# Performance work log

Hardware: AMD Instinct MI355X
Metric: run time of the kernel (lower is better)

## Reference

```python
import jax, jax.numpy as jnp
import numpy as np

N_JOINT = 12
INPUT_DIM = 4
BATCH = 524288


def _skew(w):
    z = jnp.zeros((), w.dtype)
    return jnp.stack([jnp.stack([z, -w[2], w[1]]),
                      jnp.stack([w[2], z, -w[0]]),
                      jnp.stack([-w[1], w[0], z])])


def _srodrigues(twist6, q):
    # twist6: (6,) = [rho; omega]; q: (B,) joint values -> (B,4,4) screw exponential
    rho, omega = twist6[:3], twist6[3:]
    wn = jnp.sqrt(jnp.sum(omega * omega) + 1e-12)
    u, ru = omega / wn, rho / wn
    th = q * wn                                   # (B,)
    K = _skew(u)
    K2 = K @ K
    I3 = jnp.eye(3, dtype=twist6.dtype)
    s = jnp.sin(th)[:, None, None]
    c = (1.0 - jnp.cos(th))[:, None, None]
    t = (th - jnp.sin(th))[:, None, None]
    R = I3 + s * K + c * K2                       # (B,3,3) Rodrigues rotation
    G = th[:, None, None] * I3 + c * K + t * K2   # (B,3,3) translation part
    p = G @ ru                                    # (B,3)
    top = jnp.concatenate([R, p[:, :, None]], axis=2)  # (B,3,4)
    bot = jnp.broadcast_to(jnp.array([0.0, 0.0, 0.0, 1.0], twist6.dtype), (q.shape[0], 1, 4))
    return jnp.concatenate([top, bot], axis=1)


def _rpy2r(rpy):
    r, p, y = rpy[0], rpy[1], rpy[2]
    cr, sr = jnp.cos(r), jnp.sin(r)
    cp, sp = jnp.cos(p), jnp.sin(p)
    cy, sy = jnp.cos(y), jnp.sin(y)
    return jnp.stack([
        jnp.stack([cy * cp, cy * sp * sr - sy * cr, cy * sp * cr + sy * sr]),
        jnp.stack([sy * cp, sy * sp * sr + cy * cr, sy * sp * cr - cy * sr]),
        jnp.stack([-sp, cp * sr, cp * cr])])


def _pr2t(p, rpy):
    R = _rpy2r(rpy)
    top = jnp.concatenate([R, p[:, None]], axis=1)          # (3,4)
    bot = jnp.array([[0.0, 0.0, 0.0, 1.0]], dtype=p.dtype)  # (1,4)
    return jnp.concatenate([top, bot], axis=0)


def setup_inputs() -> dict:
    key = jax.random.key(0)
    ks = jax.random.split(key, 16)
    dims = [INPUT_DIM, 16, 32, 64, 32, N_JOINT]
    inp = {"motor_control": jax.random.normal(ks[0], (BATCH, INPUT_DIM), dtype=jnp.float32)}
    for i in range(5):
        fan_in, fan_out = dims[i], dims[i + 1]
        lim = float(np.sqrt(6.0 / (fan_in + fan_out)))
        inp[f"W{i+1}"] = jax.random.uniform(ks[2 * i + 1], (fan_out, fan_in), minval=-lim, maxval=lim, dtype=jnp.float32)
        inp[f"b{i+1}"] = jax.random.uniform(ks[2 * i + 2], (fan_out,), minval=-0.1, maxval=0.1, dtype=jnp.float32)
    inp["twist"] = jax.random.uniform(ks[11], (N_JOINT, 6, 1), minval=-1.0, maxval=1.0, dtype=jnp.float32)
    inp["init_p"] = jax.random.uniform(ks[12], (1, 3, 1), minval=-1.0, maxval=1.0, dtype=jnp.float32)
    inp["init_rpy"] = jax.random.uniform(ks[13], (1, 3, 1), minval=-1.0, maxval=1.0, dtype=jnp.float32)
    return inp


def reference(motor_control, W1, b1, W2, b2, W3, b3, W4, b4, W5, b5, twist, init_p, init_rpy):
    # q_layer MLP (ReLU after every layer, including the last)
    h = jax.nn.relu(motor_control @ W1.T + b1)
    h = jax.nn.relu(h @ W2.T + b2)
    h = jax.nn.relu(h @ W3.T + b3)
    h = jax.nn.relu(h @ W4.T + b4)
    q = jax.nn.relu(h @ W5.T + b5)  # (B, n_joint)
    B = q.shape[0]
    eye4 = jnp.broadcast_to(jnp.eye(4, dtype=q.dtype), (B, 4, 4))

    def step(carry, xs):
        tw, qj = xs
        return carry @ _srodrigues(tw, qj), None

    out, _ = jax.lax.scan(step, eye4, (twist[:, :, 0], q.T))
    T0 = _pr2t(init_p[0, :, 0], init_rpy[0, :, 0])
    return out @ T0
```

## Files before the change

### kernel.cpp

```cpp
#include <hip/hip_runtime.h>
#include <math.h>

#define BATCH 524288
#define NJ 12

#define WOFF 256
#define BOFF 5632

typedef _Float16 half4 __attribute__((ext_vector_type(4)));
typedef _Float16 half2t __attribute__((ext_vector_type(2)));
typedef float f32x4 __attribute__((ext_vector_type(4)));

#define MFMA16(a, b, c) __builtin_amdgcn_mfma_f32_16x16x16f16((a), (b), (c), 0, 0, 0)

__device__ __forceinline__ f32x4 ld4(const float* p) { return *(const f32x4*)p; }

__device__ __forceinline__ void split4(f32x4 v, half4& h, half4& l) {
    half2t ha = __builtin_bit_cast(half2t, __builtin_amdgcn_cvt_pkrtz(v[0], v[1]));
    half2t hb = __builtin_bit_cast(half2t, __builtin_amdgcn_cvt_pkrtz(v[2], v[3]));
    float r0 = v[0] - (float)ha[0];
    float r1 = v[1] - (float)ha[1];
    float r2 = v[2] - (float)hb[0];
    float r3 = v[3] - (float)hb[1];
    half2t la = __builtin_bit_cast(half2t, __builtin_amdgcn_cvt_pkrtz(r0, r1));
    half2t lb = __builtin_bit_cast(half2t, __builtin_amdgcn_cvt_pkrtz(r2, r3));
    h = half4{ha[0], ha[1], hb[0], hb[1]};
    l = half4{la[0], la[1], lb[0], lb[1]};
}

__device__ __forceinline__ f32x4 relu4(f32x4 v) {
    f32x4 r;
#pragma unroll
    for (int i = 0; i < 4; i++) r[i] = fmaxf(v[i], 0.0f);
    return r;
}

__device__ __forceinline__ void unpack_frag(uint4 u, half4& h, half4& l) {
    uint2 a = make_uint2(u.x, u.y), b = make_uint2(u.z, u.w);
    h = __builtin_bit_cast(half4, a);
    l = __builtin_bit_cast(half4, b);
}

__global__ void precompute_kernel(const float* __restrict__ twist,
                                  const float* __restrict__ init_p,
                                  const float* __restrict__ init_rpy,
                                  const float* __restrict__ W1, const float* __restrict__ b1,
                                  const float* __restrict__ W2, const float* __restrict__ b2,
                                  const float* __restrict__ W3, const float* __restrict__ b3,
                                  const float* __restrict__ W4, const float* __restrict__ b4,
                                  const float* __restrict__ W5, const float* __restrict__ b5,
                                  float* __restrict__ ws) {
    const int lane = threadIdx.x;
    const int qd = lane >> 4, l16 = lane & 15;
    const f32x4 FZ = {0.f, 0.f, 0.f, 0.f};

    if (lane < NJ) {
        int j = lane;
        float rho0 = twist[j*6+0], rho1 = twist[j*6+1], rho2 = twist[j*6+2];
        float w0   = twist[j*6+3], w1   = twist[j*6+4], w2   = twist[j*6+5];
        float wn = sqrtf(w0*w0 + w1*w1 + w2*w2 + 1e-12f);
        float inv = 1.0f / wn;
        float u0 = w0*inv, u1 = w1*inv, u2 = w2*inv;
        float ru0 = rho0*inv, ru1 = rho1*inv, ru2 = rho2*inv;
        float kru0 = u1*ru2 - u2*ru1;
        float kru1 = u2*ru0 - u0*ru2;
        float kru2 = u0*ru1 - u1*ru0;
        float ud = u0*ru0 + u1*ru1 + u2*ru2;
        float* o = ws + j*20;
        o[0] = wn;  o[1] = u0;  o[2] = u1;  o[3] = u2;
        o[4] = ru0; o[5] = ru1; o[6] = ru2;
        o[7] = kru0; o[8] = kru1; o[9] = kru2;
        o[10] = u0*ud - ru0; o[11] = u1*ud - ru1; o[12] = u2*ud - ru2;
        o[13] = u0*u0; o[14] = u0*u1; o[15] = u0*u2;
        o[16] = u1*u1; o[17] = u1*u2; o[18] = u2*u2;
    } else if (lane == NJ) {
        float r = init_rpy[0], p = init_rpy[1], y = init_rpy[2];
        float cr = cosf(r), sr = sinf(r);
        float cp = cosf(p), sp = sinf(p);
        float cy = cosf(y), sy = sinf(y);
        float* o = ws + NJ*20;
        o[0] = cy*cp; o[1] = cy*sp*sr - sy*cr; o[2] = cy*sp*cr + sy*sr;
        o[3] = sy*cp; o[4] = sy*sp*sr + cy*cr; o[5] = sy*sp*cr - cy*sr;
        o[6] = -sp;   o[7] = cp*sr;            o[8] = cp*cr;
        o[9] = init_p[0]; o[10] = init_p[1]; o[11] = init_p[2];
    }

    uint4* wf = (uint4*)(ws + WOFF);
    f32x4* bf = (f32x4*)(ws + BOFF);

    auto pack = [&](f32x4 w) -> uint4 {
        half4 h, l;
#pragma unroll
        for (int i = 0; i < 4; i++) {
            _Float16 hi = (_Float16)w[i];
            h[i] = hi;
            l[i] = (_Float16)(w[i] - (float)hi);
        }
        uint2 uh = __builtin_bit_cast(uint2, h);
        uint2 ul = __builtin_bit_cast(uint2, l);
        return make_uint4(uh.x, uh.y, ul.x, ul.y);
    };

    {
        f32x4 w = ld4(W1 + l16*4);
        wf[0*64 + lane] = pack(qd == 0 ? w : FZ);
    }
    for (int ot = 0; ot < 2; ot++)
        wf[(1+ot)*64 + lane] = pack(ld4(W2 + (ot*16 + l16)*16 + 4*qd));
    for (int ot = 0; ot < 4; ot++)
        for (int kc = 0; kc < 2; kc++)
            wf[(3 + ot*2 + kc)*64 + lane] = pack(ld4(W3 + (ot*16 + l16)*32 + kc*16 + 4*qd));
    for (int ot = 0; ot < 2; ot++)
        for (int kc = 0; kc < 4; kc++)
            wf[(11 + ot*4 + kc)*64 + lane] = pack(ld4(W4 + (ot*16 + l16)*64 + kc*16 + 4*qd));
    {
        int r5 = (l16 < 12) ? l16 : 11;
        for (int kc = 0; kc < 2; kc++) {
            f32x4 w = ld4(W5 + r5*32 + kc*16 + 4*qd);
            wf[(19+kc)*64 + lane] = pack(l16 < 12 ? w : FZ);
        }
    }
    bf[0*64 + lane] = ld4(b1 + 4*qd);
    for (int ot = 0; ot < 2; ot++) bf[(1+ot)*64 + lane] = ld4(b2 + ot*16 + 4*qd);
    for (int ot = 0; ot < 4; ot++) bf[(3+ot)*64 + lane] = ld4(b3 + ot*16 + 4*qd);
    for (int ot = 0; ot < 2; ot++) bf[(7+ot)*64 + lane] = ld4(b4 + ot*16 + 4*qd);
    {
        f32x4 w = ld4(b5 + ((qd < 3) ? 4*qd : 8));
        bf[9*64 + lane] = (qd < 3) ? w : FZ;
    }
}

__global__ __launch_bounds__(256, 3) void fk_kernel(
    const float* __restrict__ mc,
    const float* __restrict__ ws,
    float* __restrict__ out) {
    const int tid = threadIdx.x;
    const int wv = tid >> 6, lane = tid & 63;
    const int qd = lane >> 4, l16 = lane & 15;
    const int wave_base = (blockIdx.x * 4 + wv) * 64;

    const uint4* wf = (const uint4*)(ws + WOFF);
    const f32x4* bf = (const f32x4*)(ws + BOFF);

    __shared__ float qbuf[4][64*13];

    f32x4 xv[4];
#pragma unroll
    for (int d = 0; d < 4; d++) {
        const int row = (d >> 1)*32 + (d & 1)*16 + l16;
        xv[d] = ld4(mc + (size_t)(wave_base + row) * 4);
    }

    const half4 HZ = {(_Float16)0, (_Float16)0, (_Float16)0, (_Float16)0};

    half4 bxh[4], bxl[4];
#pragma unroll
    for (int d = 0; d < 4; d++) {
        split4(xv[d], bxh[d], bxl[d]);
        if (qd != 0) { bxh[d] = HZ; bxl[d] = HZ; }
    }


    half4 g1h[4], g1l[4];
    {
        half4 wh, wl; unpack_frag(wf[0*64 + lane], wh, wl);
        f32x4 bv = bf[0*64 + lane];
#pragma unroll
        for (int d = 0; d < 4; d++) {
            f32x4 acc = bv;
            acc = MFMA16(wh, bxh[d], acc);
            acc = MFMA16(wh, bxl[d], acc);
            acc = MFMA16(wl, bxh[d], acc);
            split4(relu4(acc), g1h[d], g1l[d]);
        }
    }

    half4 g2h[4][2], g2l[4][2];
#pragma unroll
    for (int ot = 0; ot < 2; ot++) {
        half4 wh, wl; unpack_frag(wf[(1+ot)*64 + lane], wh, wl);
        f32x4 bv = bf[(1+ot)*64 + lane];
#pragma unroll
        for (int d = 0; d < 4; d++) {
            f32x4 acc = bv;
            acc = MFMA16(wh, g1h[d], acc);
            acc = MFMA16(wh, g1l[d], acc);
            acc = MFMA16(wl, g1h[d], acc);
            split4(relu4(acc), g2h[d][ot], g2l[d][ot]);
        }
    }

    half4 g3h[4][4], g3l[4][4];
#pragma unroll
    for (int ot = 0; ot < 4; ot++) {
        f32x4 bv = bf[(3+ot)*64 + lane];
        f32x4 acc[4];
#pragma unroll
        for (int d = 0; d < 4; d++) acc[d] = bv;
#pragma unroll
        for (int kc = 0; kc < 2; kc++) {
            half4 wh, wl; unpack_frag(wf[(3 + ot*2 + kc)*64 + lane], wh, wl);
#pragma unroll
            for (int d = 0; d < 4; d++) {
                acc[d] = MFMA16(wh, g2h[d][kc], acc[d]);
                acc[d] = MFMA16(wh, g2l[d][kc], acc[d]);
                acc[d] = MFMA16(wl, g2h[d][kc], acc[d]);
            }
        }
#pragma unroll
        for (int d = 0; d < 4; d++)
            split4(relu4(acc[d]), g3h[d][ot], g3l[d][ot]);
    }

    half4 g4h[4][2], g4l[4][2];
#pragma unroll
    for (int ot = 0; ot < 2; ot++) {
        f32x4 bv = bf[(7+ot)*64 + lane];
        f32x4 acc[4];
#pragma unroll
        for (int d = 0; d < 4; d++) acc[d] = bv;
#pragma unroll
        for (int kc = 0; kc < 4; kc++) {
            half4 wh, wl; unpack_frag(wf[(11 + ot*4 + kc)*64 + lane], wh, wl);
#pragma unroll
            for (int d = 0; d < 4; d++) {
                acc[d] = MFMA16(wh, g3h[d][kc], acc[d]);
                acc[d] = MFMA16(wh, g3l[d][kc], acc[d]);
                acc[d] = MFMA16(wl, g3h[d][kc], acc[d]);
            }
        }
#pragma unroll
        for (int d = 0; d < 4; d++)
            split4(relu4(acc[d]), g4h[d][ot], g4l[d][ot]);
    }

    {
        f32x4 bv = bf[9*64 + lane];
        f32x4 acc[4];
#pragma unroll
        for (int d = 0; d < 4; d++) acc[d] = bv;
#pragma unroll
        for (int kc = 0; kc < 2; kc++) {
            half4 wh, wl; unpack_frag(wf[(19+kc)*64 + lane], wh, wl);
#pragma unroll
            for (int d = 0; d < 4; d++) {
                acc[d] = MFMA16(wh, g4h[d][kc], acc[d]);
                acc[d] = MFMA16(wh, g4l[d][kc], acc[d]);
                acc[d] = MFMA16(wl, g4h[d][kc], acc[d]);
            }
        }
#pragma unroll
        for (int d = 0; d < 4; d++) {
            f32x4 qv = relu4(acc[d]);
            if (qd < 3) {
                const int row = (d >> 1)*32 + (d & 1)*16 + l16;
                float* qb = &qbuf[wv][row*13 + 4*qd];
                qb[0] = qv[0]; qb[1] = qv[1]; qb[2] = qv[2]; qb[3] = qv[3];
            }
        }
    }

    asm volatile("s_waitcnt lgkmcnt(0)" ::: "memory");

    float qq[12];
#pragma unroll
    for (int j = 0; j < 12; j++) qq[j] = qbuf[wv][lane*13 + j];

    const float* jc = ws;
    float M00 = 1.f, M01 = 0.f, M02 = 0.f;
    float M10 = 0.f, M11 = 1.f, M12 = 0.f;
    float M20 = 0.f, M21 = 0.f, M22 = 1.f;
    float v0 = 0.f, v1 = 0.f, v2 = 0.f;

#pragma unroll
    for (int j = 0; j < NJ; j++) {
        const float* c = jc + j*20;
        float wn = c[0];
        float u0 = c[1], u1 = c[2], u2 = c[3];
        float ru0 = c[4], ru1 = c[5], ru2 = c[6];
        float kru0 = c[7], kru1 = c[8], kru2 = c[9];
        float k2ru0 = c[10], k2ru1 = c[11], k2ru2 = c[12];
        float uu00 = c[13], uu01 = c[14], uu02 = c[15];
        float uu11 = c[16], uu12 = c[17], uu22 = c[18];

        float th = qq[j] * wn;
        float s = __sinf(th);
        float cth = __cosf(th);
        float cc = 1.0f - cth;
        float t = th - s;

        float R00 = 1.0f + cc*(uu00 - 1.0f);
        float R01 = cc*uu01 - s*u2;
        float R02 = cc*uu02 + s*u1;
        float R10 = cc*uu01 + s*u2;
        float R11 = 1.0f + cc*(uu11 - 1.0f);
        float R12 = cc*uu12 - s*u0;
        float R20 = cc*uu02 - s*u1;
        float R21 = cc*uu12 + s*u0;
        float R22 = 1.0f + cc*(uu22 - 1.0f);

        float p0 = th*ru0 + cc*kru0 + t*k2ru0;
        float p1 = th*ru1 + cc*kru1 + t*k2ru1;
        float p2 = th*ru2 + cc*kru2 + t*k2ru2;

        float n00 = M00*R00 + M01*R10 + M02*R20;
        float n01 = M00*R01 + M01*R11 + M02*R21;
        float n02 = M00*R02 + M01*R12 + M02*R22;
        float n10 = M10*R00 + M11*R10 + M12*R20;
        float n11 = M10*R01 + M11*R11 + M12*R21;
        float n12 = M10*R02 + M11*R12 + M12*R22;
        float n20 = M20*R00 + M21*R10 + M22*R20;
        float n21 = M20*R01 + M21*R11 + M22*R21;
        float n22 = M20*R02 + M21*R12 + M22*R22;
        v0 += M00*p0 + M01*p1 + M02*p2;
        v1 += M10*p0 + M11*p1 + M12*p2;
        v2 += M20*p0 + M21*p1 + M22*p2;
        M00 = n00; M01 = n01; M02 = n02;
        M10 = n10; M11 = n11; M12 = n12;
        M20 = n20; M21 = n21; M22 = n22;
    }

    const float* t0 = jc + NJ*20;
    float A00 = t0[0], A01 = t0[1], A02 = t0[2];
    float A10 = t0[3], A11 = t0[4], A12 = t0[5];
    float A20 = t0[6], A21 = t0[7], A22 = t0[8];
    float P0  = t0[9], P1  = t0[10], P2 = t0[11];

    float F00 = M00*A00 + M01*A10 + M02*A20;
    float F01 = M00*A01 + M01*A11 + M02*A21;
    float F02 = M00*A02 + M01*A12 + M02*A22;
    float F10 = M10*A00 + M11*A10 + M12*A20;
    float F11 = M10*A01 + M11*A11 + M12*A21;
    float F12 = M10*A02 + M11*A12 + M12*A22;
    float F20 = M20*A00 + M21*A10 + M22*A20;
    float F21 = M20*A01 + M21*A11 + M22*A21;
    float F22 = M20*A02 + M21*A12 + M22*A22;
    float Fv0 = M00*P0 + M01*P1 + M02*P2 + v0;
    float Fv1 = M10*P0 + M11*P1 + M12*P2 + v1;
    float Fv2 = M20*P0 + M21*P1 + M22*P2 + v2;

    const int eo = wave_base + lane;
    float4* o4 = (float4*)(out + (size_t)eo * 16);
    o4[0] = make_float4(F00, F01, F02, Fv0);
    o4[1] = make_float4(F10, F11, F12, Fv1);
    o4[2] = make_float4(F20, F21, F22, Fv2);
    o4[3] = make_float4(0.f, 0.f, 0.f, 1.f);
}

extern "C" void kernel_launch(void* const* d_in, const int* in_sizes, int n_in,
                              void* d_out, int out_size, void* d_ws, size_t ws_size,
                              hipStream_t stream) {
    const float* mc      = (const float*)d_in[0];
    const float* W1      = (const float*)d_in[1];
    const float* b1      = (const float*)d_in[2];
    const float* W2      = (const float*)d_in[3];
    const float* b2      = (const float*)d_in[4];
    const float* W3      = (const float*)d_in[5];
    const float* b3      = (const float*)d_in[6];
    const float* W4      = (const float*)d_in[7];
    const float* b4      = (const float*)d_in[8];
    const float* W5      = (const float*)d_in[9];
    const float* b5      = (const float*)d_in[10];
    const float* twist   = (const float*)d_in[11];
    const float* init_p  = (const float*)d_in[12];
    const float* init_rpy= (const float*)d_in[13];
    float* out = (float*)d_out;
    float* ws  = (float*)d_ws;

    precompute_kernel<<<1, 64, 0, stream>>>(twist, init_p, init_rpy,
                                            W1, b1, W2, b2, W3, b3, W4, b4, W5, b5, ws);
    fk_kernel<<<BATCH / 256, 256, 0, stream>>>(mc, ws, out);
}
```

Measured before the change: 129.6 us.

## Process two elements per lane with packed float2 FK chain math

Each wave now handles 128 batch elements instead of 64: the MLP runs twice in a non-unrolled loop, writing q values into a doubled shared buffer. The forward-kinematics chain then processes two elements per lane using float2 vector types, so the compiler can emit packed FP32 instructions (v_pk_fma_f32) and amortize the per-joint constant loads. The grid is halved and launch bounds lowered to 2 blocks per CU, which raises register and LDS use per wave in exchange for less occupancy.

New measurement: 128.0 us. Within noise of the previous version (-1.2%).

```diff
diff --git a/kernel.cpp b/kernel.cpp
--- a/kernel.cpp
+++ b/kernel.cpp
@@ -10,6 +10,7 @@
 typedef _Float16 half4 __attribute__((ext_vector_type(4)));
 typedef _Float16 half2t __attribute__((ext_vector_type(2)));
 typedef float f32x4 __attribute__((ext_vector_type(4)));
+typedef float f32x2 __attribute__((ext_vector_type(2)));
 
 #define MFMA16(a, b, c) __builtin_amdgcn_mfma_f32_16x16x16f16((a), (b), (c), 0, 0, 0)
 
@@ -130,147 +131,153 @@
     }
 }
 
-__global__ __launch_bounds__(256, 3) void fk_kernel(
+__global__ __launch_bounds__(256, 2) void fk_kernel(
     const float* __restrict__ mc,
     const float* __restrict__ ws,
     float* __restrict__ out) {
     const int tid = threadIdx.x;
     const int wv = tid >> 6, lane = tid & 63;
     const int qd = lane >> 4, l16 = lane & 15;
-    const int wave_base = (blockIdx.x * 4 + wv) * 64;
+    const int ebase = (blockIdx.x * 4 + wv) * 128;
 
     const uint4* wf = (const uint4*)(ws + WOFF);
     const f32x4* bf = (const f32x4*)(ws + BOFF);
 
-    __shared__ float qbuf[4][64*13];
-
-    f32x4 xv[4];
-#pragma unroll
-    for (int d = 0; d < 4; d++) {
-        const int row = (d >> 1)*32 + (d & 1)*16 + l16;
-        xv[d] = ld4(mc + (size_t)(wave_base + row) * 4);
-    }
+    __shared__ float qbuf[4][128*13];
 
     const half4 HZ = {(_Float16)0, (_Float16)0, (_Float16)0, (_Float16)0};
 
-    half4 bxh[4], bxl[4];
-#pragma unroll
-    for (int d = 0; d < 4; d++) {
-        split4(xv[d], bxh[d], bxl[d]);
-        if (qd != 0) { bxh[d] = HZ; bxl[d] = HZ; }
-    }
-
-
-    half4 g1h[4], g1l[4];
-    {
-        half4 wh, wl; unpack_frag(wf[0*64 + lane], wh, wl);
-        f32x4 bv = bf[0*64 + lane];
+#pragma unroll 1
+    for (int g = 0; g < 2; g++) {
+        f32x4 xv[4];
 #pragma unroll
         for (int d = 0; d < 4; d++) {
-            f32x4 acc = bv;
-            acc = MFMA16(wh, bxh[d], acc);
-            acc = MFMA16(wh, bxl[d], acc);
-            acc = MFMA16(wl, bxh[d], acc);
-            split4(relu4(acc), g1h[d], g1l[d]);
-        }
-    }
-
-    half4 g2h[4][2], g2l[4][2];
-#pragma unroll
-    for (int ot = 0; ot < 2; ot++) {
-        half4 wh, wl; unpack_frag(wf[(1+ot)*64 + lane], wh, wl);
-        f32x4 bv = bf[(1+ot)*64 + lane];
+            const int row = g*64 + (d >> 1)*32 + (d & 1)*16 + l16;
+            xv[d] = ld4(mc + (size_t)(ebase + row) * 4);
+        }
+
+        half4 bxh[4], bxl[4];
 #pragma unroll
         for (int d = 0; d < 4; d++) {
-            f32x4 acc = bv;
-            acc = MFMA16(wh, g1h[d], acc);
-            acc = MFMA16(wh, g1l[d], acc);
-            acc = MFMA16(wl, g1h[d], acc);
-            split4(relu4(acc), g2h[d][ot], g2l[d][ot]);
-        }
-    }
-
-    half4 g3h[4][4], g3l[4][4];
-#pragma unroll
-    for (int ot = 0; ot < 4; ot++) {
-        f32x4 bv = bf[(3+ot)*64 + lane];
-        f32x4 acc[4];
-#pragma unroll
-        for (int d = 0; d < 4; d++) acc[d] = bv;
-#pragma unroll
-        for (int kc = 0; kc < 2; kc++) {
-            half4 wh, wl; unpack_frag(wf[(3 + ot*2 + kc)*64 + lane], wh, wl);
+            split4(xv[d], bxh[d], bxl[d]);
+            if (qd != 0) { bxh[d] = HZ; bxl[d] = HZ; }
+        }
+
+
+        half4 g1h[4], g1l[4];
+        {
+            half4 wh, wl; unpack_frag(wf[0*64 + lane], wh, wl);
+            f32x4 bv = bf[0*64 + lane];
 #pragma unroll
             for (int d = 0; d < 4; d++) {
-                acc[d] = MFMA16(wh, g2h[d][kc], acc[d]);
-                acc[d] = MFMA16(wh, g2l[d][kc], acc[d]);
-                acc[d] = MFMA16(wl, g2h[d][kc], acc[d]);
-            }
-        }
-#pragma unroll
-        for (int d = 0; d < 4; d++)
-            split4(relu4(acc[d]), g3h[d][ot], g3l[d][ot]);
-    }
-
-    half4 g4h[4][2], g4l[4][2];
-#pragma unroll
-    for (int ot = 0; ot < 2; ot++) {
-        f32x4 bv = bf[(7+ot)*64 + lane];
-        f32x4 acc[4];
-#pragma unroll
-        for (int d = 0; d < 4; d++) acc[d] = bv;
-#pragma unroll
-        for (int kc = 0; kc < 4; kc++) {
-            half4 wh, wl; unpack_frag(wf[(11 + ot*4 + kc)*64 + lane], wh, wl);
+                f32x4 acc = bv;
+                acc = MFMA16(wh, bxh[d], acc);
+                acc = MFMA16(wh, bxl[d], acc);
+                acc = MFMA16(wl, bxh[d], acc);
+                split4(relu4(acc), g1h[d], g1l[d]);
+            }
+        }
+
+        half4 g2h[4][2], g2l[4][2];
+#pragma unroll
+        for (int ot = 0; ot < 2; ot++) {
+            half4 wh, wl; unpack_frag(wf[(1+ot)*64 + lane], wh, wl);
+            f32x4 bv = bf[(1+ot)*64 + lane];
 #pragma unroll
             for (int d = 0; d < 4; d++) {
-                acc[d] = MFMA16(wh, g3h[d][kc], acc[d]);
-                acc[d] = MFMA16(wh, g3l[d][kc], acc[d]);
-                acc[d] = MFMA16(wl, g3h[d][kc], acc[d]);
-            }
-        }
-#pragma unroll
-        for (int d = 0; d < 4; d++)
-            split4(relu4(acc[d]), g4h[d][ot], g4l[d][ot]);
-    }
-
-    {
-        f32x4 bv = bf[9*64 + lane];
-        f32x4 acc[4];
-#pragma unroll
-        for (int d = 0; d < 4; d++) acc[d] = bv;
-#pragma unroll
-        for (int kc = 0; kc < 2; kc++) {
-            half4 wh, wl; unpack_frag(wf[(19+kc)*64 + lane], wh, wl);
+                f32x4 acc = bv;
+                acc = MFMA16(wh, g1h[d], acc);
+                acc = MFMA16(wh, g1l[d], acc);
+                acc = MFMA16(wl, g1h[d], acc);
+                split4(relu4(acc), g2h[d][ot], g2l[d][ot]);
+            }
+        }
+
+        half4 g3h[4][4], g3l[4][4];
+#pragma unroll
+        for (int ot = 0; ot < 4; ot++) {
+            f32x4 bv = bf[(3+ot)*64 + lane];
+            f32x4 acc[4];
+#pragma unroll
+            for (int d = 0; d < 4; d++) acc[d] = bv;
+#pragma unroll
+            for (int kc = 0; kc < 2; kc++) {
+                half4 wh, wl; unpack_frag(wf[(3 + ot*2 + kc)*64 + lane], wh, wl);
+#pragma unroll
+                for (int d = 0; d < 4; d++) {
+                    acc[d] = MFMA16(wh, g2h[d][kc], acc[d]);
+                    acc[d] = MFMA16(wh, g2l[d][kc], acc[d]);
+                    acc[d] = MFMA16(wl, g2h[d][kc], acc[d]);
+                }
+            }
+#pragma unroll
+            for (int d = 0; d < 4; d++)
+                split4(relu4(acc[d]), g3h[d][ot], g3l[d][ot]);
+        }
+
+        half4 g4h[4][2], g4l[4][2];
+#pragma unroll
+        for (int ot = 0; ot < 2; ot++) {
+            f32x4 bv = bf[(7+ot)*64 + lane];
+            f32x4 acc[4];
+#pragma unroll
+            for (int d = 0; d < 4; d++) acc[d] = bv;
+#pragma unroll
+            for (int kc = 0; kc < 4; kc++) {
+                half4 wh, wl; unpack_frag(wf[(11 + ot*4 + kc)*64 + lane], wh, wl);
+#pragma unroll
+                for (int d = 0; d < 4; d++) {
+                    acc[d] = MFMA16(wh, g3h[d][kc], acc[d]);
+                    acc[d] = MFMA16(wh, g3l[d][kc], acc[d]);
+                    acc[d] = MFMA16(wl, g3h[d][kc], acc[d]);
+                }
+            }
+#pragma unroll
+            for (int d = 0; d < 4; d++)
+                split4(relu4(acc[d]), g4h[d][ot], g4l[d][ot]);
+        }
+
+        {
+            f32x4 bv = bf[9*64 + lane];
+            f32x4 acc[4];
+#pragma unroll
+            for (int d = 0; d < 4; d++) acc[d] = bv;
+#pragma unroll
+            for (int kc = 0; kc < 2; kc++) {
+                half4 wh, wl; unpack_frag(wf[(19+kc)*64 + lane], wh, wl);
+#pragma unroll
+                for (int d = 0; d < 4; d++) {
+                    acc[d] = MFMA16(wh, g4h[d][kc], acc[d]);
+                    acc[d] = MFMA16(wh, g4l[d][kc], acc[d]);
+                    acc[d] = MFMA16(wl, g4h[d][kc], acc[d]);
+                }
+            }
 #pragma unroll
             for (int d = 0; d < 4; d++) {
-                acc[d] = MFMA16(wh, g4h[d][kc], acc[d]);
-                acc[d] = MFMA16(wh, g4l[d][kc], acc[d]);
-                acc[d] = MFMA16(wl, g4h[d][kc], acc[d]);
-            }
-        }
-#pragma unroll
-        for (int d = 0; d < 4; d++) {
-            f32x4 qv = relu4(acc[d]);
-            if (qd < 3) {
-                const int row = (d >> 1)*32 + (d & 1)*16 + l16;
-                float* qb = &qbuf[wv][row*13 + 4*qd];
-                qb[0] = qv[0]; qb[1] = qv[1]; qb[2] = qv[2]; qb[3] = qv[3];
+                f32x4 qv = relu4(acc[d]);
+                if (qd < 3) {
+                    const int row = g*64 + (d >> 1)*32 + (d & 1)*16 + l16;
+                    float* qb = &qbuf[wv][row*13 + 4*qd];
+                    qb[0] = qv[0]; qb[1] = qv[1]; qb[2] = qv[2]; qb[3] = qv[3];
+                }
             }
         }
     }
 
     asm volatile("s_waitcnt lgkmcnt(0)" ::: "memory");
 
-    float qq[12];
-#pragma unroll
-    for (int j = 0; j < 12; j++) qq[j] = qbuf[wv][lane*13 + j];
+    f32x2 qq[12];
+#pragma unroll
+    for (int j = 0; j < 12; j++) {
+        qq[j] = f32x2{ qbuf[wv][lane*13 + j], qbuf[wv][(64 + lane)*13 + j] };
+    }
 
     const float* jc = ws;
-    float M00 = 1.f, M01 = 0.f, M02 = 0.f;
-    float M10 = 0.f, M11 = 1.f, M12 = 0.f;
-    float M20 = 0.f, M21 = 0.f, M22 = 1.f;
-    float v0 = 0.f, v1 = 0.f, v2 = 0.f;
+    const f32x2 ONE2 = {1.f, 1.f}, Z2 = {0.f, 0.f};
+    f32x2 M00 = ONE2, M01 = Z2, M02 = Z2;
+    f32x2 M10 = Z2, M11 = ONE2, M12 = Z2;
+    f32x2 M20 = Z2, M21 = Z2, M22 = ONE2;
+    f32x2 v0 = Z2, v1 = Z2, v2 = Z2;
 
 #pragma unroll
     for (int j = 0; j < NJ; j++) {
@@ -283,35 +290,38 @@
         float uu00 = c[13], uu01 = c[14], uu02 = c[15];
         float uu11 = c[16], uu12 = c[17], uu22 = c[18];
 
-        float th = qq[j] * wn;
-        float s = __sinf(th);
-        float cth = __cosf(th);
-        float cc = 1.0f - cth;
-        float t = th - s;
-
-        float R00 = 1.0f + cc*(uu00 - 1.0f);
-        float R01 = cc*uu01 - s*u2;
-        float R02 = cc*uu02 + s*u1;
-        float R10 = cc*uu01 + s*u2;
-        float R11 = 1.0f + cc*(uu11 - 1.0f);
-        float R12 = cc*uu12 - s*u0;
-        float R20 = cc*uu02 - s*u1;
-        float R21 = cc*uu12 + s*u0;
-        float R22 = 1.0f + cc*(uu22 - 1.0f);
-
-        float p0 = th*ru0 + cc*kru0 + t*k2ru0;
-        float p1 = th*ru1 + cc*kru1 + t*k2ru1;
-        float p2 = th*ru2 + cc*kru2 + t*k2ru2;
-
-        float n00 = M00*R00 + M01*R10 + M02*R20;
-        float n01 = M00*R01 + M01*R11 + M02*R21;
-        float n02 = M00*R02 + M01*R12 + M02*R22;
-        float n10 = M10*R00 + M11*R10 + M12*R20;
-        float n11 = M10*R01 + M11*R11 + M12*R21;
-        float n12 = M10*R02 + M11*R12 + M12*R22;
-        float n20 = M20*R00 + M21*R10 + M22*R20;
-        float n21 = M20*R01 + M21*R11 + M22*R21;
-        float n22 = M20*R02 + M21*R12 + M22*R22;
+        f32x2 th = qq[j] * wn;
+        f32x2 s, cth;
+        s.x = __sinf(th.x);
+        s.y = __sinf(th.y);
+        cth.x = __cosf(th.x);
+        cth.y = __cosf(th.y);
+        f32x2 cc = 1.0f - cth;
+        f32x2 t = th - s;
+
+        f32x2 R00 = 1.0f + cc*(uu00 - 1.0f);
+        f32x2 R01 = cc*uu01 - s*u2;
+        f32x2 R02 = cc*uu02 + s*u1;
+        f32x2 R10 = cc*uu01 + s*u2;
+        f32x2 R11 = 1.0f + cc*(uu11 - 1.0f);
+        f32x2 R12 = cc*uu12 - s*u0;
+        f32x2 R20 = cc*uu02 - s*u1;
+        f32x2 R21 = cc*uu12 + s*u0;
+        f32x2 R22 = 1.0f + cc*(uu22 - 1.0f);
+
+        f32x2 p0 = th*ru0 + cc*kru0 + t*k2ru0;
+        f32x2 p1 = th*ru1 + cc*kru1 + t*k2ru1;
+        f32x2 p2 = th*ru2 + cc*kru2 + t*k2ru2;
+
+        f32x2 n00 = M00*R00 + M01*R10 + M02*R20;
+        f32x2 n01 = M00*R01 + M01*R11 + M02*R21;
+        f32x2 n02 = M00*R02 + M01*R12 + M02*R22;
+        f32x2 n10 = M10*R00 + M11*R10 + M12*R20;
+        f32x2 n11 = M10*R01 + M11*R11 + M12*R21;
+        f32x2 n12 = M10*R02 + M11*R12 + M12*R22;
+        f32x2 n20 = M20*R00 + M21*R10 + M22*R20;
+        f32x2 n21 = M20*R01 + M21*R11 + M22*R21;
+        f32x2 n22 = M20*R02 + M21*R12 + M22*R22;
         v0 += M00*p0 + M01*p1 + M02*p2;
         v1 += M10*p0 + M11*p1 + M12*p2;
         v2 += M20*p0 + M21*p1 + M22*p2;
@@ -326,25 +336,35 @@
     float A20 = t0[6], A21 = t0[7], A22 = t0[8];
     float P0  = t0[9], P1  = t0[10], P2 = t0[11];
 
-    float F00 = M00*A00 + M01*A10 + M02*A20;
-    float F01 = M00*A01 + M01*A11 + M02*A21;
-    float F02 = M00*A02 + M01*A12 + M02*A22;
-    float F10 = M10*A00 + M11*A10 + M12*A20;
-    float F11 = M10*A01 + M11*A11 + M12*A21;
-    float F12 = M10*A02 + M11*A12 + M12*A22;
-    float F20 = M20*A00 + M21*A10 + M22*A20;
-    float F21 = M20*A01 + M21*A11 + M22*A21;
-    float F22 = M20*A02 + M21*A12 + M22*A22;
-    float Fv0 = M00*P0 + M01*P1 + M02*P2 + v0;
-    float Fv1 = M10*P0 + M11*P1 + M12*P2 + v1;
-    float Fv2 = M20*P0 + M21*P1 + M22*P2 + v2;
-
-    const int eo = wave_base + lane;
-    float4* o4 = (float4*)(out + (size_t)eo * 16);
-    o4[0] = make_float4(F00, F01, F02, Fv0);
-    o4[1] = make_float4(F10, F11, F12, Fv1);
-    o4[2] = make_float4(F20, F21, F22, Fv2);
-    o4[3] = make_float4(0.f, 0.f, 0.f, 1.f);
+    f32x2 F00 = M00*A00 + M01*A10 + M02*A20;
+    f32x2 F01 = M00*A01 + M01*A11 + M02*A21;
+    f32x2 F02 = M00*A02 + M01*A12 + M02*A22;
+    f32x2 F10 = M10*A00 + M11*A10 + M12*A20;
+    f32x2 F11 = M10*A01 + M11*A11 + M12*A21;
+    f32x2 F12 = M10*A02 + M11*A12 + M12*A22;
+    f32x2 F20 = M20*A00 + M21*A10 + M22*A20;
+    f32x2 F21 = M20*A01 + M21*A11 + M22*A21;
+    f32x2 F22 = M20*A02 + M21*A12 + M22*A22;
+    f32x2 Fv0 = M00*P0 + M01*P1 + M02*P2 + v0;
+    f32x2 Fv1 = M10*P0 + M11*P1 + M12*P2 + v1;
+    f32x2 Fv2 = M20*P0 + M21*P1 + M22*P2 + v2;
+
+    {
+        const int e0 = ebase + lane;
+        float4* o4 = (float4*)(out + (size_t)e0 * 16);
+        o4[0] = make_float4(F00.x, F01.x, F02.x, Fv0.x);
+        o4[1] = make_float4(F10.x, F11.x, F12.x, Fv1.x);
+        o4[2] = make_float4(F20.x, F21.x, F22.x, Fv2.x);
+        o4[3] = make_float4(0.f, 0.f, 0.f, 1.f);
+    }
+    {
+        const int e1 = ebase + 64 + lane;
+        float4* o4 = (float4*)(out + (size_t)e1 * 16);
+        o4[0] = make_float4(F00.y, F01.y, F02.y, Fv0.y);
+        o4[1] = make_float4(F10.y, F11.y, F12.y, Fv1.y);
+        o4[2] = make_float4(F20.y, F21.y, F22.y, Fv2.y);
+        o4[3] = make_float4(0.f, 0.f, 0.f, 1.f);
+    }
 }
 
 extern "C" void kernel_launch(void* const* d_in, const int* in_sizes, int n_in,
@@ -369,5 +389,5 @@
 
     precompute_kernel<<<1, 64, 0, stream>>>(twist, init_p, init_rpy,
                                             W1, b1, W2, b2, W3, b3, W4, b4, W5, b5, ws);
-    fk_kernel<<<BATCH / 256, 256, 0, stream>>>(mc, ws, out);
-}
+    fk_kernel<<<BATCH / 512, 256, 0, stream>>>(mc, ws, out);
+}
```
